# Kernel optimization log

Hardware: AMD Instinct MI355X
Metric: run time of the kernel (lower is better)

## Reference

```python
import jax, jax.numpy as jnp
import numpy as np

B, T, D, H, E, K = 4, 2048, 512, 1024, 8, 2


def setup_inputs() -> dict:
    key = jax.random.key(0)
    ks = jax.random.split(key, 6)
    x = jax.random.normal(ks[0], (B, T, D), dtype=jnp.float32)
    Wg = jax.random.normal(ks[1], (D, E), dtype=jnp.float32) / np.sqrt(D)  # gate (no bias)
    W1 = jax.random.normal(ks[2], (E, D, H), dtype=jnp.float32) / np.sqrt(D)
    b1 = jnp.zeros((E, H), dtype=jnp.float32)
    W2 = jax.random.normal(ks[3], (E, H, D), dtype=jnp.float32) / np.sqrt(H)
    b2 = jnp.zeros((E, D), dtype=jnp.float32)
    return {"x": x, "Wg": Wg, "W1": W1, "b1": b1, "W2": W2, "b2": b2}


def reference(x, Wg, W1, b1, W2, b2):
    # Dropout is identity at inference (p applied only in train mode).
    Bx, Tx, Dx = x.shape
    N = Bx * Tx
    xf = x.reshape(N, Dx)

    # --- Router: top-k over gate logits, softmax over the k selected logits ---
    router_logits = xf @ Wg                               # [N, E]
    topk_logits, topk_idx = jax.lax.top_k(router_logits, K)  # [N, K]
    topk_w = jax.nn.softmax(topk_logits, axis=-1)         # [N, K]

    # Dense combine weights: combine[n, e] = sum of topk weights routing token n to expert e
    combine = jnp.zeros((N, E), dtype=x.dtype).at[
        jnp.arange(N)[:, None], topk_idx
    ].add(topk_w)                                         # [N, E]

    # --- Experts (batched over E): GELU(x W1 + b1) W2 + b2 ---
    h = jax.nn.gelu(jnp.einsum('nd,edh->enh', xf, W1) + b1[:, None, :],
                    approximate=False)                    # [E, N, H]
    y = jnp.einsum('enh,ehd->end', h, W2) + b2[:, None, :]  # [E, N, D]

    # --- Combine: weighted sum of expert outputs per token ---
    out = jnp.einsum('end,ne->nd', y, combine).reshape(Bx, Tx, Dx)

    aux_logits = router_logits.reshape(Bx, Tx, E)
    aux_idx = topk_idx.reshape(Bx, Tx, K)
    aux_w = topk_w.reshape(Bx, Tx, K)
    return out, aux_logits, aux_idx, aux_w
```

## Files before the change

kernel.cpp:

```cpp
#include <hip/hip_runtime.h>
#include <hip/hip_bf16.h>

#define NTOK 8192
#define DDIM 512
#define HDIM 1024
#define NEXP 8
#define TOPK 2

typedef __attribute__((ext_vector_type(8))) short short8;
typedef __attribute__((ext_vector_type(4))) float f32x4;

__device__ __forceinline__ short f2bf(float f) {
  union { float f; unsigned u; } v; v.f = f;
  unsigned r = v.u + 0x7fffu + ((v.u >> 16) & 1u);
  return (short)(r >> 16);
}
__device__ __forceinline__ float bf2f(short s) {
  union { unsigned u; float f; } v; v.u = ((unsigned)(unsigned short)s) << 16;
  return v.f;
}

__device__ __forceinline__ void async_lds16(const void* g, void* l) {
  __builtin_amdgcn_global_load_lds(
      (const __attribute__((address_space(1))) unsigned int*)g,
      (__attribute__((address_space(3))) unsigned int*)l,
      16, 0, 0);
}

__device__ __forceinline__ float gelu_f(float v) {
  float u = v * (0.7978845608f + 0.0356774081f * v * v);
  float t = __expf(-2.f * fabsf(u));
  float th = __builtin_copysignf((1.f - t) / (1.f + t), u);
  return 0.5f * v * (1.f + th);
}

__global__ __launch_bounds__(256) void transpose_bf16_kernel(const float* __restrict__ src,
                                                             short* __restrict__ dst,
                                                             int R, int C) {
  __shared__ float tile[32][33];
  int m = blockIdx.z;
  int c0 = blockIdx.x * 32, r0 = blockIdx.y * 32;
  const float* s = src + (size_t)m * R * C;
  short* d = dst + (size_t)m * R * C;
  int tx = threadIdx.x, ty = threadIdx.y;
#pragma unroll
  for (int i = 0; i < 4; ++i)
    tile[ty + i * 8][tx] = s[(size_t)(r0 + ty + i * 8) * C + c0 + tx];
  __syncthreads();
#pragma unroll
  for (int i = 0; i < 4; ++i)
    d[(size_t)(c0 + ty + i * 8) * R + r0 + tx] = f2bf(tile[tx][ty + i * 8]);
}

__global__ __launch_bounds__(256) void router_compute(
    const float* __restrict__ x, const float* __restrict__ wg,
    float* __restrict__ out_logits, float* __restrict__ out_idx,
    float* __restrict__ out_w, short* __restrict__ xb) {
  int wave = threadIdx.x >> 6;
  int lane = threadIdx.x & 63;
  int n = blockIdx.x * 4 + wave;

  const float* xrow = x + (size_t)n * DDIM;
  const float4* xv = (const float4*)xrow;
  float4 xa = xv[lane * 2], xbv = xv[lane * 2 + 1];
  float xs[8] = {xa.x, xa.y, xa.z, xa.w, xbv.x, xbv.y, xbv.z, xbv.w};

  short8 xc;
#pragma unroll
  for (int j = 0; j < 8; ++j) xc[j] = f2bf(xs[j]);
  *(short8*)(xb + (size_t)n * DDIM + lane * 8) = xc;

  float acc[8] = {0, 0, 0, 0, 0, 0, 0, 0};
#pragma unroll
  for (int j = 0; j < 8; ++j) {
    const float4* wr = (const float4*)(wg + (size_t)(lane * 8 + j) * NEXP);
    float4 w0 = wr[0], w1 = wr[1];
    float xj = xs[j];
    acc[0] += xj * w0.x; acc[1] += xj * w0.y; acc[2] += xj * w0.z; acc[3] += xj * w0.w;
    acc[4] += xj * w1.x; acc[5] += xj * w1.y; acc[6] += xj * w1.z; acc[7] += xj * w1.w;
  }
#pragma unroll
  for (int m = 32; m >= 1; m >>= 1) {
#pragma unroll
    for (int e = 0; e < 8; ++e) acc[e] += __shfl_xor(acc[e], m);
  }
  if (lane == 0) {
#pragma unroll
    for (int e = 0; e < 8; ++e) out_logits[(size_t)n * NEXP + e] = acc[e];
    int i1 = 0; float v1 = acc[0];
#pragma unroll
    for (int e = 1; e < 8; ++e) if (acc[e] > v1) { v1 = acc[e]; i1 = e; }
    int i2 = -1; float v2 = -3.4e38f;
#pragma unroll
    for (int e = 0; e < 8; ++e) if (e != i1 && acc[e] > v2) { v2 = acc[e]; i2 = e; }
    float ex = expf(v2 - v1);
    float s = 1.f / (1.f + ex);
    out_idx[n * 2] = (float)i1; out_idx[n * 2 + 1] = (float)i2;
    out_w[n * 2] = s; out_w[n * 2 + 1] = ex * s;
  }
}

__global__ __launch_bounds__(512) void build_lists(
    const float* __restrict__ idxf,
    int* __restrict__ counts, int* __restrict__ tok_list, int* __restrict__ slot_enc) {
  int t = blockIdx.x * 512 + threadIdx.x;
  int lane = threadIdx.x & 63;
  float2 iv = *(const float2*)(idxf + (size_t)t * 2);
  int es[2] = {(int)iv.x, (int)iv.y};
#pragma unroll
  for (int s = 0; s < 2; ++s) {
    int e = es[s];
#pragma unroll
    for (int ex = 0; ex < NEXP; ++ex) {
      unsigned long long m = __ballot(e == ex);
      if (e == ex) {
        int leader = __ffsll(m) - 1;
        int base = 0;
        if (lane == leader) base = atomicAdd(&counts[ex], __popcll(m));
        base = __shfl(base, leader);
        int rank = __popcll(m & ((1ull << lane) - 1ull));
        tok_list[ex * NTOK + base + rank] = t;
        slot_enc[t * 2 + s] = (ex << 16) | (base + rank);
      }
    }
  }
}

__global__ __launch_bounds__(256) void expert_gemm1(
    const short* __restrict__ xb, const short* __restrict__ w1t,
    const float* __restrict__ b1, short* __restrict__ hbuf,
    const int* __restrict__ ctrl, const int* __restrict__ tok_list) {
  int raw = blockIdx.x;
  int bid = (raw & 7) * 512 + (raw >> 3);
  int e = bid >> 9;
  int rem = bid & 511;
  int mt = rem >> 3;
  int nt = rem & 7;
  int ce = ctrl[e];
  int m0 = mt * 128;
  if (m0 >= ce) return;
  int offe = 0;
#pragma unroll
  for (int i = 0; i < NEXP; ++i) offe += (i < e) ? ctrl[i] : 0;

  __shared__ char smem[34816];

  int tid = threadIdx.x;
  int wave = tid >> 6;
  int lane = tid & 63;

  int sr = tid >> 2;
  int kc = (tid & 3) * 8;
  int ia = m0 + sr;      if (ia >= ce) ia = ce - 1;
  int ib = m0 + sr + 64; if (ib >= ce) ib = ce - 1;
  const short* gA0 = xb + (size_t)tok_list[e * NTOK + ia] * DDIM + kc;
  const short* gA1 = xb + (size_t)tok_list[e * NTOK + ib] * DDIM + kc;
  const short* gB0 = w1t + ((size_t)e * HDIM + nt * 128 + sr) * DDIM + kc;
  const short* gB1 = gB0 + (size_t)64 * DDIM;

  f32x4 acc[4][4];
#pragma unroll
  for (int i = 0; i < 4; ++i)
#pragma unroll
    for (int j = 0; j < 4; ++j) acc[i][j] = (f32x4){0.f, 0.f, 0.f, 0.f};

  int wm = (wave >> 1) * 64;
  int wn = (wave & 1) * 64;
  int lr = lane & 15;
  int kh = (lane >> 4) * 8;

#define STAGE1(t) do {                                                  \
    int _k = (t) * 32;                                                  \
    char* _lA = smem + (((t) & 1) << 14) + wave * 1024;                 \
    char* _lB = _lA + 8192;                                             \
    async_lds16(gA0 + _k, _lA); async_lds16(gA1 + _k, _lA + 4096);      \
    async_lds16(gB0 + _k, _lB); async_lds16(gB1 + _k, _lB + 4096);      \
  } while (0)

  STAGE1(0);
#pragma unroll
  for (int t = 0; t < 16; ++t) {
    __syncthreads();
    if (t < 15) STAGE1(t + 1);
    const short* As = (const short*)(smem + ((t & 1) << 14));
    const short* Bs = As + 4096;
    short8 a[4], b[4];
#pragma unroll
    for (int i = 0; i < 4; ++i) a[i] = *(const short8*)&As[(wm + i * 16 + lr) * 32 + kh];
#pragma unroll
    for (int j = 0; j < 4; ++j) b[j] = *(const short8*)&Bs[(wn + j * 16 + lr) * 32 + kh];
#pragma unroll
    for (int i = 0; i < 4; ++i)
#pragma unroll
      for (int j = 0; j < 4; ++j)
        acc[i][j] = __builtin_amdgcn_mfma_f32_16x16x32_bf16(a[i], b[j], acc[i][j], 0, 0, 0);
  }
#undef STAGE1
  __syncthreads();

  short* ep = (short*)(smem + wave * 8704);
  int colb = nt * 128 + wn;
#pragma unroll
  for (int j = 0; j < 4; ++j) {
    int colH = colb + j * 16 + lr;
    float bb = b1[e * HDIM + colH];
#pragma unroll
    for (int i = 0; i < 4; ++i) {
#pragma unroll
      for (int q = 0; q < 4; ++q) {
        int rl = i * 16 + (lane >> 4) * 4 + q;
        ep[rl * 68 + j * 16 + lr] = f2bf(gelu_f(acc[i][j][q] + bb));
      }
    }
  }
  __syncthreads();
#pragma unroll
  for (int s = 0; s < 8; ++s) {
    int idx = s * 64 + lane;
    int rl = idx >> 3;
    int c8 = (idx & 7) * 8;
    int gidx = m0 + wm + rl;
    if (gidx < ce) {
      *(short8*)&hbuf[(size_t)(offe + gidx) * HDIM + colb + c8] = *(short8*)&ep[rl * 68 + c8];
    }
  }
}

__global__ __launch_bounds__(256) void expert_gemm2(
    const short* __restrict__ hbuf, const short* __restrict__ w2t,
    const float* __restrict__ b2, short* __restrict__ ybuf,
    const int* __restrict__ ctrl) {
  int raw = blockIdx.x;
  int bid = (raw & 7) * 256 + (raw >> 3);
  int e = bid >> 8;
  int rem = bid & 255;
  int mt = rem >> 2;
  int nt = rem & 3;
  int ce = ctrl[e];
  int m0 = mt * 128;
  if (m0 >= ce) return;
  int offe = 0;
#pragma unroll
  for (int i = 0; i < NEXP; ++i) offe += (i < e) ? ctrl[i] : 0;

  __shared__ char smem[34816];

  int tid = threadIdx.x;
  int wave = tid >> 6;
  int lane = tid & 63;

  int sr = tid >> 2;
  int kc = (tid & 3) * 8;
  int ia = m0 + sr;      if (ia >= ce) ia = ce - 1;
  int ib = m0 + sr + 64; if (ib >= ce) ib = ce - 1;
  const short* gA0 = hbuf + (size_t)(offe + ia) * HDIM + kc;
  const short* gA1 = hbuf + (size_t)(offe + ib) * HDIM + kc;
  const short* gB0 = w2t + ((size_t)e * DDIM + nt * 128 + sr) * HDIM + kc;
  const short* gB1 = gB0 + (size_t)64 * HDIM;

  f32x4 acc[4][4];
#pragma unroll
  for (int i = 0; i < 4; ++i)
#pragma unroll
    for (int j = 0; j < 4; ++j) acc[i][j] = (f32x4){0.f, 0.f, 0.f, 0.f};

  int wm = (wave >> 1) * 64;
  int wn = (wave & 1) * 64;
  int lr = lane & 15;
  int kh = (lane >> 4) * 8;

#define STAGE2(t) do {                                                  \
    int _k = (t) * 32;                                                  \
    char* _lA = smem + (((t) & 1) << 14) + wave * 1024;                 \
    char* _lB = _lA + 8192;                                             \
    async_lds16(gA0 + _k, _lA); async_lds16(gA1 + _k, _lA + 4096);      \
    async_lds16(gB0 + _k, _lB); async_lds16(gB1 + _k, _lB + 4096);      \
  } while (0)

  STAGE2(0);
#pragma unroll
  for (int t = 0; t < 32; ++t) {
    __syncthreads();
    if (t < 31) STAGE2(t + 1);
    const short* As = (const short*)(smem + ((t & 1) << 14));
    const short* Bs = As + 4096;
    short8 a[4], b[4];
#pragma unroll
    for (int i = 0; i < 4; ++i) a[i] = *(const short8*)&As[(wm + i * 16 + lr) * 32 + kh];
#pragma unroll
    for (int j = 0; j < 4; ++j) b[j] = *(const short8*)&Bs[(wn + j * 16 + lr) * 32 + kh];
#pragma unroll
    for (int i = 0; i < 4; ++i)
#pragma unroll
      for (int j = 0; j < 4; ++j)
        acc[i][j] = __builtin_amdgcn_mfma_f32_16x16x32_bf16(a[i], b[j], acc[i][j], 0, 0, 0);
  }
#undef STAGE2
  __syncthreads();

  short* ep = (short*)(smem + wave * 8704);
  int colb = nt * 128 + wn;
#pragma unroll
  for (int j = 0; j < 4; ++j) {
    int colD = colb + j * 16 + lr;
    float bb = b2[e * DDIM + colD];
#pragma unroll
    for (int i = 0; i < 4; ++i) {
#pragma unroll
      for (int q = 0; q < 4; ++q) {
        int rl = i * 16 + (lane >> 4) * 4 + q;
        ep[rl * 68 + j * 16 + lr] = f2bf(acc[i][j][q] + bb);
      }
    }
  }
  __syncthreads();
#pragma unroll
  for (int s = 0; s < 8; ++s) {
    int idx = s * 64 + lane;
    int rl = idx >> 3;
    int c8 = (idx & 7) * 8;
    int gidx = m0 + wm + rl;
    if (gidx < ce) {
      *(short8*)&ybuf[(size_t)(offe + gidx) * DDIM + colb + c8] = *(short8*)&ep[rl * 68 + c8];
    }
  }
}

__global__ __launch_bounds__(256) void combine_kernel(
    const short* __restrict__ ybuf, const int* __restrict__ slot_enc,
    const float* __restrict__ wf, const int* __restrict__ ctrl,
    float* __restrict__ out) {
  int wave = threadIdx.x >> 6;
  int lane = threadIdx.x & 63;
  int n = blockIdx.x * 4 + wave;
  int s0 = slot_enc[n * 2], s1 = slot_enc[n * 2 + 1];
  float w0 = wf[n * 2], w1 = wf[n * 2 + 1];
  int e0 = s0 >> 16, e1 = s1 >> 16;
  int off0 = 0, off1 = 0;
#pragma unroll
  for (int i = 0; i < NEXP; ++i) {
    int c = ctrl[i];
    off0 += (i < e0) ? c : 0;
    off1 += (i < e1) ? c : 0;
  }
  int r0 = off0 + (s0 & 0xffff);
  int r1 = off1 + (s1 & 0xffff);
  short8 a = *(const short8*)&ybuf[(size_t)r0 * DDIM + lane * 8];
  short8 b = *(const short8*)&ybuf[(size_t)r1 * DDIM + lane * 8];
  float r[8];
#pragma unroll
  for (int k = 0; k < 8; ++k) r[k] = w0 * bf2f(a[k]) + w1 * bf2f(b[k]);
  float4 o0 = {r[0], r[1], r[2], r[3]};
  float4 o1 = {r[4], r[5], r[6], r[7]};
  *(float4*)&out[(size_t)n * DDIM + lane * 8] = o0;
  *(float4*)&out[(size_t)n * DDIM + lane * 8 + 4] = o1;
}

extern "C" void kernel_launch(void* const* d_in, const int* in_sizes, int n_in,
                              void* d_out, int out_size, void* d_ws, size_t ws_size,
                              hipStream_t stream) {
  const float* x  = (const float*)d_in[0];
  const float* wg = (const float*)d_in[1];
  const float* w1 = (const float*)d_in[2];
  const float* b1 = (const float*)d_in[3];
  const float* w2 = (const float*)d_in[4];
  const float* b2 = (const float*)d_in[5];
  float* out = (float*)d_out;

  char* ws = (char*)d_ws;
  int*   ctrl = (int*)ws;
  int*   tok  = (int*)(ws + 1024);
  int*   slot = (int*)(ws + 263168);
  short* xb   = (short*)(ws + 328704);
  short* w1t  = (short*)(ws + 8717312);
  short* w2t  = (short*)(ws + 17105920);
  short* hb   = (short*)(ws + 25494528);
  short* yb   = (short*)(ws + 328704);

  hipMemsetAsync(d_ws, 0, 1024, stream);

  transpose_bf16_kernel<<<dim3(32, 16, 8), dim3(32, 8), 0, stream>>>(w1, w1t, DDIM, HDIM);
  transpose_bf16_kernel<<<dim3(16, 32, 8), dim3(32, 8), 0, stream>>>(w2, w2t, HDIM, DDIM);

  float* out_logits = out + (size_t)NTOK * DDIM;
  float* out_idx = out_logits + (size_t)NTOK * NEXP;
  float* out_w = out_idx + (size_t)NTOK * TOPK;
  router_compute<<<2048, 256, 0, stream>>>(x, wg, out_logits, out_idx, out_w, xb);
  build_lists<<<16, 512, 0, stream>>>(out_idx, ctrl, tok, slot);

  expert_gemm1<<<4096, 256, 0, stream>>>(xb, w1t, b1, hb, ctrl, tok);
  expert_gemm2<<<2048, 256, 0, stream>>>(hb, w2t, b2, yb, ctrl);
  combine_kernel<<<2048, 256, 0, stream>>>(yb, slot, out_w, ctrl, out);
}
```

Baseline: 138.0 us.

## Triple-buffer LDS tiles in expert GEMMs with partial vmcnt waits

Both expert GEMM kernels move from double to triple buffering of the LDS A/B tiles, issuing global-to-LDS loads two K-steps ahead. The full __syncthreads is replaced by an explicit s_waitcnt vmcnt(4) plus s_barrier, so only the oldest stage must land before compute. Wave priority is also raised around the MFMA block. This is meant to hide global load latency behind MFMA work, at the cost of more LDS per block (48KB), which may lower occupancy.

Result: no change. 139.8 us (+1.3%).

```diff
diff --git a/kernel.cpp b/kernel.cpp
--- a/kernel.cpp
+++ b/kernel.cpp
@@ -143,7 +143,7 @@
 #pragma unroll
   for (int i = 0; i < NEXP; ++i) offe += (i < e) ? ctrl[i] : 0;
 
-  __shared__ char smem[34816];
+  __shared__ char smem[49152];
 
   int tid = threadIdx.x;
   int wave = tid >> 6;
@@ -171,29 +171,36 @@
 
 #define STAGE1(t) do {                                                  \
     int _k = (t) * 32;                                                  \
-    char* _lA = smem + (((t) & 1) << 14) + wave * 1024;                 \
+    char* _lA = smem + ((t) % 3) * 16384 + wave * 1024;                 \
     char* _lB = _lA + 8192;                                             \
     async_lds16(gA0 + _k, _lA); async_lds16(gA1 + _k, _lA + 4096);      \
     async_lds16(gB0 + _k, _lB); async_lds16(gB1 + _k, _lB + 4096);      \
   } while (0)
 
   STAGE1(0);
+  STAGE1(1);
 #pragma unroll
   for (int t = 0; t < 16; ++t) {
-    __syncthreads();
-    if (t < 15) STAGE1(t + 1);
-    const short* As = (const short*)(smem + ((t & 1) << 14));
+    if (t < 15) asm volatile("s_waitcnt vmcnt(4)\n\ts_barrier" ::: "memory");
+    else        asm volatile("s_waitcnt vmcnt(0)\n\ts_barrier" ::: "memory");
+    __builtin_amdgcn_sched_barrier(0);
+    if (t + 2 < 16) STAGE1(t + 2);
+    const short* As = (const short*)(smem + (t % 3) * 16384);
     const short* Bs = As + 4096;
     short8 a[4], b[4];
 #pragma unroll
     for (int i = 0; i < 4; ++i) a[i] = *(const short8*)&As[(wm + i * 16 + lr) * 32 + kh];
 #pragma unroll
     for (int j = 0; j < 4; ++j) b[j] = *(const short8*)&Bs[(wn + j * 16 + lr) * 32 + kh];
+    asm volatile("s_waitcnt lgkmcnt(0)" ::: "memory");
+    __builtin_amdgcn_sched_barrier(0);
+    __builtin_amdgcn_s_setprio(1);
 #pragma unroll
     for (int i = 0; i < 4; ++i)
 #pragma unroll
       for (int j = 0; j < 4; ++j)
         acc[i][j] = __builtin_amdgcn_mfma_f32_16x16x32_bf16(a[i], b[j], acc[i][j], 0, 0, 0);
+    __builtin_amdgcn_s_setprio(0);
   }
 #undef STAGE1
   __syncthreads();
@@ -243,7 +250,7 @@
 #pragma unroll
   for (int i = 0; i < NEXP; ++i) offe += (i < e) ? ctrl[i] : 0;
 
-  __shared__ char smem[34816];
+  __shared__ char smem[49152];
 
   int tid = threadIdx.x;
   int wave = tid >> 6;
@@ -271,29 +278,36 @@
 
 #define STAGE2(t) do {                                                  \
     int _k = (t) * 32;                                                  \
-    char* _lA = smem + (((t) & 1) << 14) + wave * 1024;                 \
+    char* _lA = smem + ((t) % 3) * 16384 + wave * 1024;                 \
     char* _lB = _lA + 8192;                                             \
     async_lds16(gA0 + _k, _lA); async_lds16(gA1 + _k, _lA + 4096);      \
     async_lds16(gB0 + _k, _lB); async_lds16(gB1 + _k, _lB + 4096);      \
   } while (0)
 
   STAGE2(0);
+  STAGE2(1);
 #pragma unroll
   for (int t = 0; t < 32; ++t) {
-    __syncthreads();
-    if (t < 31) STAGE2(t + 1);
-    const short* As = (const short*)(smem + ((t & 1) << 14));
+    if (t < 31) asm volatile("s_waitcnt vmcnt(4)\n\ts_barrier" ::: "memory");
+    else        asm volatile("s_waitcnt vmcnt(0)\n\ts_barrier" ::: "memory");
+    __builtin_amdgcn_sched_barrier(0);
+    if (t + 2 < 32) STAGE2(t + 2);
+    const short* As = (const short*)(smem + (t % 3) * 16384);
     const short* Bs = As + 4096;
     short8 a[4], b[4];
 #pragma unroll
     for (int i = 0; i < 4; ++i) a[i] = *(const short8*)&As[(wm + i * 16 + lr) * 32 + kh];
 #pragma unroll
     for (int j = 0; j < 4; ++j) b[j] = *(const short8*)&Bs[(wn + j * 16 + lr) * 32 + kh];
+    asm volatile("s_waitcnt lgkmcnt(0)" ::: "memory");
+    __builtin_amdgcn_sched_barrier(0);
+    __builtin_amdgcn_s_setprio(1);
 #pragma unroll
     for (int i = 0; i < 4; ++i)
 #pragma unroll
       for (int j = 0; j < 4; ++j)
         acc[i][j] = __builtin_amdgcn_mfma_f32_16x16x32_bf16(a[i], b[j], acc[i][j], 0, 0, 0);
+    __builtin_amdgcn_s_setprio(0);
   }
 #undef STAGE2
   __syncthreads();
```
